# Kernel tuning notes

Measured on AMD Instinct MI355X. Metric: run time of the kernel, lower is better.

The kernel has to match this reference:

```python
import jax, jax.numpy as jnp
import numpy as np

B, N, D = 64, 256, 1024
E_T, E_C, TOP_K = 4, 4, 2
E = E_T + E_C
HT = 4 * N      # token-mixer hidden
HC = 4 * D      # channel-mixer hidden
HM = 4 * D      # mlp hidden
EPS = 1e-6


def _ln(x):
    mu = jnp.mean(x, axis=-1, keepdims=True)
    var = jnp.mean(jnp.square(x - mu), axis=-1, keepdims=True)
    return (x - mu) * jax.lax.rsqrt(var + EPS)


def _gelu(x):
    return jax.nn.gelu(x, approximate=True)


def _modulate(x, shift, scale):
    return x * (1.0 + scale[:, None, :]) + shift[:, None, :]


def setup_inputs() -> dict:
    key = jax.random.key(0)
    ks = jax.random.split(key, 20)
    def rn(k, shape, fan_in):
        return (jax.random.normal(k, shape, dtype=jnp.float32) / np.sqrt(fan_in)).astype(jnp.float32)
    return {
        "x": jax.random.normal(ks[0], (B, N, D), dtype=jnp.float32),
        "c": jax.random.normal(ks[1], (B, D), dtype=jnp.float32),
        "w_ada": rn(ks[2], (D, 6 * D), D),
        "b_ada": jnp.zeros((6 * D,), jnp.float32),
        "w_router": rn(ks[3], (D, E), D),
        "tm_w1": rn(ks[4], (E_T, N, HT), N),
        "tm_b1": jnp.zeros((E_T, HT), jnp.float32),
        "tm_w2": rn(ks[5], (E_T, HT, N), HT),
        "tm_b2": jnp.zeros((E_T, N), jnp.float32),
        "cm_w1": rn(ks[6], (E_C, D, HC), D),
        "cm_b1": jnp.zeros((E_C, HC), jnp.float32),
        "cm_w2": rn(ks[7], (E_C, HC, D), HC),
        "cm_b2": jnp.zeros((E_C, D), jnp.float32),
        "mlp_w1": rn(ks[8], (D, HM), D),
        "mlp_b1": jnp.zeros((HM,), jnp.float32),
        "mlp_w2": rn(ks[9], (HM, D), HM),
        "mlp_b2": jnp.zeros((D,), jnp.float32),
    }


def _mixer(h, w_router, tm_w1, tm_b1, tm_w2, tm_b2, cm_w1, cm_b1, cm_w2, cm_b2):
    # per-sample routing on mean-pooled tokens
    r_in = jnp.mean(h, axis=1)                         # (B, D)
    logits = r_in @ w_router                            # (B, E)
    probs = jax.nn.softmax(logits, axis=-1)
    tw, ti = jax.lax.top_k(probs, TOP_K)                # (B, K)
    tw = tw / jnp.sum(tw, axis=-1, keepdims=True)
    # combine weights: (B, E), zero for non-selected experts
    combine = jnp.zeros((h.shape[0], E), h.dtype).at[jnp.arange(h.shape[0])[:, None], ti].add(tw)
    out = jnp.zeros_like(h)
    hT = jnp.swapaxes(h, 1, 2)                          # (B, D, N)
    for e in range(E_T):
        hid = _gelu(jnp.einsum('bdn,nh->bdh', hT, tm_w1[e]) + tm_b1[e])
        oe = jnp.einsum('bdh,hn->bdn', hid, tm_w2[e]) + tm_b2[e]
        out = out + combine[:, e, None, None] * jnp.swapaxes(oe, 1, 2)
    for e in range(E_C):
        hid = _gelu(jnp.einsum('bnd,dh->bnh', h, cm_w1[e]) + cm_b1[e])
        oe = jnp.einsum('bnh,hd->bnd', hid, cm_w2[e]) + cm_b2[e]
        out = out + combine[:, E_T + e, None, None] * oe
    # aux load-balancing loss (top-1 assignment fraction x mean probs)
    frac = jnp.mean(jax.nn.one_hot(ti[:, 0], E, dtype=probs.dtype), axis=0)
    aux = E * jnp.sum(jnp.mean(probs, axis=0) * frac)
    return out, aux


def reference(x, c, w_ada, b_ada, w_router, tm_w1, tm_b1, tm_w2, tm_b2,
              cm_w1, cm_b1, cm_w2, cm_b2, mlp_w1, mlp_b1, mlp_w2, mlp_b2):
    mod = jax.nn.silu(c) @ w_ada + b_ada                # (B, 6D)
    s_msa, sc_msa, g_msa, s_mlp, sc_mlp, g_mlp = jnp.split(mod, 6, axis=1)
    h = _modulate(_ln(x), s_msa, sc_msa)
    mix, aux = _mixer(h, w_router, tm_w1, tm_b1, tm_w2, tm_b2, cm_w1, cm_b1, cm_w2, cm_b2)
    x = x + g_msa[:, None, :] * mix
    h2 = _modulate(_ln(x), s_mlp, sc_mlp)
    m = _gelu(h2 @ mlp_w1 + mlp_b1) @ mlp_w2 + mlp_b2
    x = x + g_mlp[:, None, :] * m
    return x, aux
```

## Files before the change

kernel.cpp:

```cpp
#include <hip/hip_runtime.h>
#include <stdint.h>

typedef unsigned short u16;
typedef __attribute__((ext_vector_type(8))) __bf16 bf16x8;
typedef __attribute__((ext_vector_type(4))) float f32x4;

#define DEV static __device__ __forceinline__

#define VMW8 asm volatile("s_waitcnt vmcnt(8)" ::: "memory")
#define VMW4 asm volatile("s_waitcnt vmcnt(4)" ::: "memory")
#define VMW0 asm volatile("s_waitcnt vmcnt(0)" ::: "memory")
#define LGK0 asm volatile("s_waitcnt lgkmcnt(0)" ::: "memory")

DEV u16 f2b(float f) {
  uint32_t u = __builtin_bit_cast(uint32_t, f);
  u += 0x7fffu + ((u >> 16) & 1u);
  return (u16)(u >> 16);
}
DEV float gelu_f(float x) {
  return 0.5f * x * (1.0f + tanhf(0.7978845608028654f * (x + 0.044715f * x * x * x)));
}
DEV void async_cp16(const void* g, void* l) {
  __builtin_amdgcn_global_load_lds(
      (const __attribute__((address_space(1))) unsigned int*)g,
      (__attribute__((address_space(3))) unsigned int*)l, 16, 0, 0);
}

DEV int xcd_work(void) {
  int nwg = gridDim.x * gridDim.y;
  int hid = blockIdx.x + blockIdx.y * gridDim.x;
  int cpx = nwg >> 3;
  return (hid & 7) * cpx + (hid >> 3);
}

DEV void gemm_tile(const u16* __restrict__ A, int lda,
                   const u16* __restrict__ B, int ldb, int K,
                   u16* As, u16* Bs, f32x4 acc[4][4]) {
  const int tid = threadIdx.x;
  const int w = tid >> 6;
  const int L = tid & 63;
  const int sr = L >> 2;
  const int sk = (L & 3) * 8;
  const int fm = L & 15;
  const int fk = (L >> 4) * 8;
  const u16* ga0 = A + (size_t)(w * 32 + sr) * lda + sk;
  const u16* ga1 = ga0 + 16 * (size_t)lda;
  const u16* gb0 = B + (size_t)(w * 32 + sr) * ldb + sk;
  const u16* gb1 = gb0 + 16 * (size_t)ldb;
  const int lofs = w * 1024 + L * 8;
  const int nst = K >> 5;

  VMW0;
  __syncthreads();

  {
    u16* la = As + lofs; u16* lb = Bs + lofs;
    async_cp16(ga0, la); async_cp16(ga1, la + 512);
    async_cp16(gb0, lb); async_cp16(gb1, lb + 512);
    la += 4096; lb += 4096;
    async_cp16(ga0 + 32, la); async_cp16(ga1 + 32, la + 512);
    async_cp16(gb0 + 32, lb); async_cp16(gb1 + 32, lb + 512);
  }
  int s0 = 0, s1 = 4096, s2 = 8192;
  for (int t = 0; t < nst; ++t) {
    if (t + 2 < nst) {
      const int kt = (t + 2) * 32;
      u16* la = As + s2 + lofs; u16* lb = Bs + s2 + lofs;
      async_cp16(ga0 + kt, la); async_cp16(ga1 + kt, la + 512);
      async_cp16(gb0 + kt, lb); async_cp16(gb1 + kt, lb + 512);
      VMW8;
    } else if (t + 1 < nst) {
      VMW4;
    } else {
      VMW0;
    }
    __builtin_amdgcn_s_barrier();
    const u16* fa = As + s0 + ((w & 1) * 64 + fm) * 32 + fk;
    const u16* fb = Bs + s0 + ((w >> 1) * 64 + fm) * 32 + fk;
    bf16x8 av[4], bv[4];
#pragma unroll
    for (int i = 0; i < 4; ++i) {
      av[i] = *(const bf16x8*)(fa + i * 512);
      bv[i] = *(const bf16x8*)(fb + i * 512);
    }
#pragma unroll
    for (int i = 0; i < 4; ++i)
#pragma unroll
      for (int j = 0; j < 4; ++j)
        acc[i][j] = __builtin_amdgcn_mfma_f32_16x16x32_bf16(av[i], bv[j], acc[i][j], 0, 0, 0);
    LGK0;
    __builtin_amdgcn_s_barrier();
    __builtin_amdgcn_sched_barrier(0);
    const int tmp = s0; s0 = s1; s1 = s2; s2 = tmp;
  }
}

DEV void zero_acc(f32x4 acc[4][4]) {
  f32x4 z = {0.f, 0.f, 0.f, 0.f};
#pragma unroll
  for (int i = 0; i < 4; ++i)
#pragma unroll
    for (int j = 0; j < 4; ++j) acc[i][j] = z;
}

__global__ void k_diag(float* out, float v) {
  if (threadIdx.x == 0 && blockIdx.x == 0) out[0] = v;
}

struct TDesc { const float* src; long dstOff; int R, C, tileStart, tilesX; };
struct TArgs { TDesc d[17]; int n; };

__global__ __launch_bounds__(256) void k_transpose(TArgs a, u16* __restrict__ ws) {
  __shared__ float tl[32][33];
  int bid = blockIdx.x;
  int di = 0;
  for (int i = 1; i < a.n; ++i) di = (bid >= a.d[i].tileStart) ? i : di;
  TDesc dd = a.d[di];
  int lt = bid - dd.tileStart;
  int tx = lt % dd.tilesX, ty = lt / dd.tilesX;
  int cc = threadIdx.x & 31, rr = threadIdx.x >> 5;
  const float* sp = dd.src + (size_t)(ty * 32) * dd.C + tx * 32;
#pragma unroll
  for (int i = 0; i < 4; ++i) tl[rr + 8 * i][cc] = sp[(size_t)(rr + 8 * i) * dd.C + cc];
  __syncthreads();
  u16* dp = ws + dd.dstOff + (size_t)(tx * 32) * dd.R + ty * 32;
#pragma unroll
  for (int i = 0; i < 4; ++i) dp[(size_t)(rr + 8 * i) * dd.R + cc] = f2b(tl[cc][rr + 8 * i]);
}

__global__ __launch_bounds__(256) void k_silu(const float* __restrict__ c, u16* __restrict__ cs) {
  int row = blockIdx.x, t = threadIdx.x;
  float4 v = {0.f, 0.f, 0.f, 0.f};
  if (row < 64) v = ((const float4*)(c + (size_t)row * 1024))[t];
  ushort4 o;
  o.x = f2b(v.x / (1.f + expf(-v.x)));
  o.y = f2b(v.y / (1.f + expf(-v.y)));
  o.z = f2b(v.z / (1.f + expf(-v.z)));
  o.w = f2b(v.w / (1.f + expf(-v.w)));
  ((ushort4*)(cs + (size_t)row * 1024))[t] = o;
}

__global__ __launch_bounds__(256) void k_ada(const u16* __restrict__ cs, const u16* __restrict__ wT,
                                             const float* __restrict__ bada, float* __restrict__ modp) {
  __shared__ u16 As[12288] __attribute__((aligned(16)));
  __shared__ u16 Bs[12288] __attribute__((aligned(16)));
  int tn = blockIdx.x;
  f32x4 acc[4][4]; zero_acc(acc);
  gemm_tile(cs, 1024, wT + (size_t)tn * 131072, 1024, 1024, As, Bs, acc);
  const int tid = threadIdx.x, w = tid >> 6, L = tid & 63;
  const int rb = (w & 1) * 64 + ((L >> 4) << 2), cb = (w >> 1) * 64 + (L & 15);
#pragma unroll
  for (int i = 0; i < 4; ++i)
#pragma unroll
    for (int j = 0; j < 4; ++j) {
      int col = tn * 128 + cb + j * 16;
      float bv = bada[col];
#pragma unroll
      for (int r = 0; r < 4; ++r) {
        int row = rb + i * 16 + r;
        modp[(size_t)row * 6144 + col] = acc[i][j][r] + bv;
      }
    }
}

__global__ __launch_bounds__(256) void k_ln(const float* __restrict__ xin, const float* __restrict__ modp,
                                            u16* __restrict__ hout, float* __restrict__ stats,
                                            int shOff, int scOff) {
  int n = blockIdx.x, b = blockIdx.y, t = threadIdx.x;
  const float* xr = xin + ((size_t)b * 256 + n) * 1024;
  float4 v = ((const float4*)xr)[t];
  float s = v.x + v.y + v.z + v.w;
  float s2 = v.x * v.x + v.y * v.y + v.z * v.z + v.w * v.w;
#pragma unroll
  for (int o = 32; o; o >>= 1) { s += __shfl_down(s, o); s2 += __shfl_down(s2, o); }
  __shared__ float red[8];
  int wv = t >> 6, l = t & 63;
  if (l == 0) { red[wv] = s; red[4 + wv] = s2; }
  __syncthreads();
  float S = red[0] + red[1] + red[2] + red[3];
  float S2 = red[4] + red[5] + red[6] + red[7];
  float mu = S * (1.f / 1024.f);
  float var = S2 * (1.f / 1024.f) - mu * mu;
  float rstd = rsqrtf(var + 1e-6f);
  if (stats != nullptr && t == 0) { stats[b * 256 + n] = mu; stats[16384 + b * 256 + n] = rstd; }
  float4 sh = ((const float4*)(modp + b * 6144 + shOff))[t];
  float4 sc = ((const float4*)(modp + b * 6144 + scOff))[t];
  ushort4 o;
  o.x = f2b(((v.x - mu) * rstd) * (1.f + sc.x) + sh.x);
  o.y = f2b(((v.y - mu) * rstd) * (1.f + sc.y) + sh.y);
  o.z = f2b(((v.z - mu) * rstd) * (1.f + sc.z) + sh.z);
  o.w = f2b(((v.w - mu) * rstd) * (1.f + sc.w) + sh.w);
  ((ushort4*)(hout + ((size_t)b * 256 + n) * 1024))[t] = o;
}

__global__ __launch_bounds__(256) void k_htrans(const u16* __restrict__ h, u16* __restrict__ hT) {
  __shared__ u16 tl[32][33];
  int b = blockIdx.z, d0 = blockIdx.x * 32, n0 = blockIdx.y * 32;
  int c = threadIdx.x & 31, r = threadIdx.x >> 5;
  const u16* src = h + (size_t)b * 262144;
#pragma unroll
  for (int i = 0; i < 4; ++i) tl[r + 8 * i][c] = src[(size_t)(n0 + r + 8 * i) * 1024 + d0 + c];
  __syncthreads();
  u16* dst = hT + (size_t)b * 262144;
#pragma unroll
  for (int i = 0; i < 4; ++i) dst[(size_t)(d0 + r + 8 * i) * 256 + n0 + c] = tl[c][r + 8 * i];
}

__global__ __launch_bounds__(256) void k_rin(const float* __restrict__ x, const float* __restrict__ lns,
                                             const float* __restrict__ modp, float* __restrict__ rin) {
  int b = blockIdx.y, d = blockIdx.x * 256 + threadIdx.x;
  const float* xp = x + (size_t)b * 262144 + d;
  const float* mu = lns + b * 256;
  const float* rs = lns + 16384 + b * 256;
  float s = 0.f;
  for (int n = 0; n < 256; ++n) s += (xp[(size_t)n * 1024] - mu[n]) * rs[n];
  float sc = modp[b * 6144 + 1024 + d], sh = modp[b * 6144 + d];
  rin[b * 1024 + d] = (1.f + sc) * (s * (1.f / 256.f)) + sh;
}

__global__ __launch_bounds__(256) void k_router(const float* __restrict__ rin, const float* __restrict__ wr,
                                                float* __restrict__ probs, float* __restrict__ tw,
                                                int* __restrict__ ti, int* __restrict__ top1) {
  __shared__ float red[256][8];
  int b = blockIdx.x, t = threadIdx.x;
  float a[8];
#pragma unroll
  for (int e = 0; e < 8; ++e) a[e] = 0.f;
  for (int d = t; d < 1024; d += 256) {
    float rv = rin[b * 1024 + d];
    const float* wp = wr + d * 8;
#pragma unroll
    for (int e = 0; e < 8; ++e) a[e] += rv * wp[e];
  }
#pragma unroll
  for (int e = 0; e < 8; ++e) red[t][e] = a[e];
  __syncthreads();
  for (int s = 128; s > 0; s >>= 1) {
    if (t < s)
#pragma unroll
      for (int e = 0; e < 8; ++e) red[t][e] += red[t + s][e];
    __syncthreads();
  }
  if (t == 0) {
    float p[8];
    float m = -1e30f;
    for (int e = 0; e < 8; ++e) m = fmaxf(m, red[0][e]);
    float sum = 0.f;
    for (int e = 0; e < 8; ++e) { p[e] = expf(red[0][e] - m); sum += p[e]; }
    float inv = 1.f / sum;
    for (int e = 0; e < 8; ++e) p[e] *= inv;
    int i1 = 0;
    for (int e = 1; e < 8; ++e) if (p[e] > p[i1]) i1 = e;
    int i2 = -1; float bv = -1e30f;
    for (int e = 0; e < 8; ++e) if (e != i1 && p[e] > bv) { bv = p[e]; i2 = e; }
    float ss = p[i1] + p[i2];
    ti[b * 2] = i1; ti[b * 2 + 1] = i2;
    tw[b * 2] = p[i1] / ss; tw[b * 2 + 1] = p[i2] / ss;
    top1[b] = i1;
    for (int e = 0; e < 8; ++e) probs[b * 8 + e] = p[e];
  }
}

__global__ void k_aux(const float* __restrict__ probs, const int* __restrict__ top1,
                      float* __restrict__ auxout) {
  if (threadIdx.x != 0) return;
  float mp[8], fr[8];
  for (int e = 0; e < 8; ++e) { mp[e] = 0.f; fr[e] = 0.f; }
  for (int b = 0; b < 64; ++b) {
    for (int e = 0; e < 8; ++e) mp[e] += probs[b * 8 + e];
    fr[top1[b]] += 1.f;
  }
  float aux = 0.f;
  for (int e = 0; e < 8; ++e) aux += (mp[e] * (1.f / 64.f)) * (fr[e] * (1.f / 64.f));
  auxout[0] = 8.f * aux;
}

__global__ __launch_bounds__(256) void k_gemm1(const u16* __restrict__ h, const u16* __restrict__ hT,
                                               const u16* __restrict__ tmw1T, const u16* __restrict__ cmw1T,
                                               const float* __restrict__ tm_b1, const float* __restrict__ cm_b1,
                                               const int* __restrict__ ti, u16* __restrict__ hid, int slot0) {
  __shared__ u16 As[12288] __attribute__((aligned(16)));
  __shared__ u16 Bs[12288] __attribute__((aligned(16)));
  const int wrk = xcd_work();
  int tile = wrk & 63;
  int ly = wrk >> 6;
  int slot = slot0 + ly;
  int b = slot >> 1;
  int e = ti[slot];
  f32x4 acc[4][4]; zero_acc(acc);
  const int tid = threadIdx.x, w = tid >> 6, L = tid & 63;
  const int rb = (w & 1) * 64 + ((L >> 4) << 2), cb = (w >> 1) * 64 + (L & 15);
  u16* outp = hid + (size_t)ly * 1048576;
  if (e < 4) {
    int tm = tile >> 3, tn = tile & 7;
    gemm_tile(hT + (size_t)b * 262144 + (size_t)tm * 128 * 256, 256,
              tmw1T + (size_t)e * 262144 + (size_t)tn * 128 * 256, 256, 256, As, Bs, acc);
    const float* bias = tm_b1 + e * 1024 + tn * 128;
#pragma unroll
    for (int i = 0; i < 4; ++i)
#pragma unroll
      for (int j = 0; j < 4; ++j) {
        int col = cb + j * 16;
        float bv = bias[col];
#pragma unroll
        for (int r = 0; r < 4; ++r) {
          int row = tm * 128 + rb + i * 16 + r;
          outp[(size_t)row * 1024 + tn * 128 + col] = f2b(gelu_f(acc[i][j][r] + bv));
        }
      }
  } else {
    int ec = e - 4;
    int tm = tile >> 5, tn = tile & 31;
    gemm_tile(h + (size_t)b * 262144 + (size_t)tm * 128 * 1024, 1024,
              cmw1T + (size_t)ec * 4194304 + (size_t)tn * 128 * 1024, 1024, 1024, As, Bs, acc);
    const float* bias = cm_b1 + ec * 4096 + tn * 128;
#pragma unroll
    for (int i = 0; i < 4; ++i)
#pragma unroll
      for (int j = 0; j < 4; ++j) {
        int col = cb + j * 16;
        float bv = bias[col];
#pragma unroll
        for (int r = 0; r < 4; ++r) {
          int row = tm * 128 + rb + i * 16 + r;
          outp[(size_t)row * 4096 + tn * 128 + col] = f2b(gelu_f(acc[i][j][r] + bv));
        }
      }
  }
}

__global__ __launch_bounds__(256) void k_gemm2(const u16* __restrict__ hid,
                                               const u16* __restrict__ tmw2T, const u16* __restrict__ cmw2T,
                                               const float* __restrict__ tm_b2, const float* __restrict__ cm_b2,
                                               const int* __restrict__ ti, const float* __restrict__ tw,
                                               const float* __restrict__ x, const float* __restrict__ modp,
                                               float* __restrict__ x1, int b0) {
  __shared__ u16 As[12288] __attribute__((aligned(16)));
  __shared__ u16 Bs[12288] __attribute__((aligned(16)));
  const int wrk = xcd_work();
  int tm = (wrk & 15) >> 3, tn = wrk & 7;
  int ly = wrk >> 4;
  int b = b0 + ly;
  int e0 = ti[b * 2], e1 = ti[b * 2 + 1];
  float w0 = tw[b * 2], w1v = tw[b * 2 + 1];
  f32x4 acc[4][4]; zero_acc(acc);
  const int tid = threadIdx.x, w = tid >> 6, L = tid & 63;
  const int rb = (w & 1) * 64 + ((L >> 4) << 2), cb = (w >> 1) * 64 + (L & 15);
  const u16* hid0 = hid + (size_t)(2 * ly) * 1048576;
  const u16* hid1 = hid0 + 1048576;
  if (e0 < 4)
    gemm_tile(tmw2T + (size_t)e0 * 262144 + (size_t)tm * 128 * 1024, 1024,
              hid0 + (size_t)tn * 128 * 1024, 1024, 1024, As, Bs, acc);
  else
    gemm_tile(hid0 + (size_t)tm * 128 * 4096, 4096,
              cmw2T + (size_t)(e0 - 4) * 4194304 + (size_t)tn * 128 * 4096, 4096, 4096, As, Bs, acc);
  float ratio = w0 / w1v;
#pragma unroll
  for (int i = 0; i < 4; ++i)
#pragma unroll
    for (int j = 0; j < 4; ++j)
#pragma unroll
      for (int r = 0; r < 4; ++r) {
        int rowg = tm * 128 + rb + i * 16 + r;
        int colg = tn * 128 + cb + j * 16;
        float bv = (e0 < 4) ? tm_b2[e0 * 256 + rowg] : cm_b2[(e0 - 4) * 1024 + colg];
        acc[i][j][r] = (acc[i][j][r] + bv) * ratio;
      }
  if (e1 < 4)
    gemm_tile(tmw2T + (size_t)e1 * 262144 + (size_t)tm * 128 * 1024, 1024,
              hid1 + (size_t)tn * 128 * 1024, 1024, 1024, As, Bs, acc);
  else
    gemm_tile(hid1 + (size_t)tm * 128 * 4096, 4096,
              cmw2T + (size_t)(e1 - 4) * 4194304 + (size_t)tn * 128 * 4096, 4096, 4096, As, Bs, acc);
  const float* xrow = x + (size_t)b * 262144;
  const float* gm = modp + b * 6144 + 2048;
  float* orow = x1 + (size_t)b * 262144;
#pragma unroll
  for (int i = 0; i < 4; ++i)
#pragma unroll
    for (int j = 0; j < 4; ++j)
#pragma unroll
      for (int r = 0; r < 4; ++r) {
        int rowg = tm * 128 + rb + i * 16 + r;
        int colg = tn * 128 + cb + j * 16;
        float bv = (e1 < 4) ? tm_b2[e1 * 256 + rowg] : cm_b2[(e1 - 4) * 1024 + colg];
        float val = w1v * (acc[i][j][r] + bv);
        size_t idx = (size_t)rowg * 1024 + colg;
        orow[idx] = xrow[idx] + gm[colg] * val;
      }
}

__global__ __launch_bounds__(256) void k_mlp1(const u16* __restrict__ h2, const u16* __restrict__ w1T,
                                              const float* __restrict__ b1, u16* __restrict__ mhid, int r0) {
  __shared__ u16 As[12288] __attribute__((aligned(16)));
  __shared__ u16 Bs[12288] __attribute__((aligned(16)));
  const int wrk = xcd_work();
  int tn = wrk & 31, tm = wrk >> 5;
  f32x4 acc[4][4]; zero_acc(acc);
  gemm_tile(h2 + (size_t)(r0 + tm * 128) * 1024, 1024, w1T + (size_t)tn * 131072, 1024, 1024, As, Bs, acc);
  const int tid = threadIdx.x, w = tid >> 6, L = tid & 63;
  const int rb = (w & 1) * 64 + ((L >> 4) << 2), cb = (w >> 1) * 64 + (L & 15);
  const float* bias = b1 + tn * 128;
#pragma unroll
  for (int i = 0; i < 4; ++i)
#pragma unroll
    for (int j = 0; j < 4; ++j) {
      int col = cb + j * 16;
      float bv = bias[col];
#pragma unroll
      for (int r = 0; r < 4; ++r) {
        int row = tm * 128 + rb + i * 16 + r;
        mhid[(size_t)row * 4096 + tn * 128 + col] = f2b(gelu_f(acc[i][j][r] + bv));
      }
    }
}

__global__ __launch_bounds__(256) void k_mlp2(const u16* __restrict__ mhid, const u16* __restrict__ w2T,
                                              const float* __restrict__ b2, const float* __restrict__ modp,
                                              float* __restrict__ xio, int r0) {
  __shared__ u16 As[12288] __attribute__((aligned(16)));
  __shared__ u16 Bs[12288] __attribute__((aligned(16)));
  const int wrk = xcd_work();
  int tn = wrk & 7, tm = wrk >> 3;
  f32x4 acc[4][4]; zero_acc(acc);
  gemm_tile(mhid + (size_t)tm * 524288, 4096, w2T + (size_t)tn * 524288, 4096, 4096, As, Bs, acc);
  const int tid = threadIdx.x, w = tid >> 6, L = tid & 63;
  const int rb = (w & 1) * 64 + ((L >> 4) << 2), cb = (w >> 1) * 64 + (L & 15);
#pragma unroll
  for (int i = 0; i < 4; ++i)
#pragma unroll
    for (int j = 0; j < 4; ++j) {
      int col = tn * 128 + cb + j * 16;
      float bv = b2[col];
#pragma unroll
      for (int r = 0; r < 4; ++r) {
        int gr = r0 + tm * 128 + rb + i * 16 + r;
        int bq = gr >> 8;
        size_t idx = (size_t)gr * 1024 + col;
        xio[idx] = xio[idx] + modp[bq * 6144 + 5120 + col] * (acc[i][j][r] + bv);
      }
    }
}

extern "C" void kernel_launch(void* const* d_in, const int* in_sizes, int n_in,
                              void* d_out, int out_size, void* d_ws, size_t ws_size,
                              hipStream_t stream) {
  (void)in_sizes; (void)n_in; (void)out_size;
  const float* x        = (const float*)d_in[0];
  const float* c        = (const float*)d_in[1];
  const float* w_ada    = (const float*)d_in[2];
  const float* b_ada    = (const float*)d_in[3];
  const float* w_router = (const float*)d_in[4];
  const float* tm_w1    = (const float*)d_in[5];
  const float* tm_b1    = (const float*)d_in[6];
  const float* tm_w2    = (const float*)d_in[7];
  const float* tm_b2    = (const float*)d_in[8];
  const float* cm_w1    = (const float*)d_in[9];
  const float* cm_b1    = (const float*)d_in[10];
  const float* cm_w2    = (const float*)d_in[11];
  const float* cm_b2    = (const float*)d_in[12];
  const float* mlp_w1   = (const float*)d_in[13];
  const float* mlp_b1   = (const float*)d_in[14];
  const float* mlp_w2   = (const float*)d_in[15];
  const float* mlp_b2   = (const float*)d_in[16];

  u16* ws16 = (u16*)d_ws;
  char* wsb = (char*)d_ws;
  u16* tmw1T = ws16;
  u16* tmw2T = ws16 + 1048576L;
  u16* cmw1T = ws16 + 2097152L;
  u16* cmw2T = ws16 + 18874368L;
  u16* csilu = ws16 + 35651584L;
  u16* h     = ws16 + 35782656L;
  u16* hT    = ws16 + 52559872L;
  u16* mw1T  = ws16 + 52559872L;
  u16* mw2T  = ws16 + 56754176L;
  float* modp  = (float*)(wsb + 138674176L);
  float* rin   = (float*)(wsb + 141819904L);
  float* probs = (float*)(wsb + 142082048L);
  float* twp   = (float*)(wsb + 142084096L);
  int*   tip   = (int*)(wsb + 142084608L);
  int*   top1p = (int*)(wsb + 142085120L);
  float* lns   = (float*)(wsb + 142085376L);
  const size_t FIXED_END = 142216448ULL;
  u16* tailb = ws16 + FIXED_END / 2;
  float* x1 = (float*)d_out;

  if (ws_size < FIXED_END + 12582912ULL) {
    k_diag<<<1, 64, 0, stream>>>((float*)d_out, (float)(ws_size >> 20));
    return;
  }
  size_t tail = ws_size - FIXED_END;
  int C = 64;
  while ((size_t)C * 4194304ULL > tail) C >>= 1;
  int R = 16384;
  while ((size_t)R * 8192ULL > tail) R >>= 1;

  TArgs t1; int k = 0, start = 0;
#define ADD_T(TA, SRC, DST, RR, CC)                                       \
  do {                                                                    \
    TA.d[k].src = (SRC); TA.d[k].dstOff = (DST);                          \
    TA.d[k].R = (RR); TA.d[k].C = (CC);                                   \
    TA.d[k].tileStart = start; TA.d[k].tilesX = (CC) / 32;                \
    start += ((RR) / 32) * ((CC) / 32); ++k;                              \
  } while (0)
  ADD_T(t1, w_ada, (long)(FIXED_END / 2), 1024, 6144);
  for (int e = 0; e < 4; ++e) ADD_T(t1, tm_w1 + (long)e * 262144, 0L + (long)e * 262144, 256, 1024);
  for (int e = 0; e < 4; ++e) ADD_T(t1, tm_w2 + (long)e * 262144, 1048576L + (long)e * 262144, 1024, 256);
  for (int e = 0; e < 4; ++e) ADD_T(t1, cm_w1 + (long)e * 4194304, 2097152L + (long)e * 4194304, 1024, 4096);
  for (int e = 0; e < 4; ++e) ADD_T(t1, cm_w2 + (long)e * 4194304, 18874368L + (long)e * 4194304, 4096, 1024);
  t1.n = k;
  int t1_tiles = start;

  TArgs t2; k = 0; start = 0;
  ADD_T(t2, mlp_w1, 52559872L, 1024, 4096);
  ADD_T(t2, mlp_w2, 56754176L, 4096, 1024);
  t2.n = k;
  int t2_tiles = start;
#undef ADD_T

  k_transpose<<<dim3(t1_tiles), dim3(256), 0, stream>>>(t1, ws16);
  k_silu<<<dim3(128), dim3(256), 0, stream>>>(c, csilu);
  k_ada<<<dim3(48), dim3(256), 0, stream>>>(csilu, tailb, b_ada, modp);
  k_ln<<<dim3(256, 64), dim3(256), 0, stream>>>(x, modp, h, lns, 0, 1024);
  k_htrans<<<dim3(32, 8, 64), dim3(256), 0, stream>>>(h, hT);
  k_rin<<<dim3(4, 64), dim3(256), 0, stream>>>(x, lns, modp, rin);
  k_router<<<dim3(64), dim3(256), 0, stream>>>(rin, w_router, probs, twp, tip, top1p);
  k_aux<<<dim3(1), dim3(64), 0, stream>>>(probs, top1p, (float*)d_out + 16777216L);
  for (int b0 = 0; b0 < 64; b0 += C) {
    k_gemm1<<<dim3(64, 2 * C), dim3(256), 0, stream>>>(h, hT, tmw1T, cmw1T, tm_b1, cm_b1, tip, tailb, 2 * b0);
    k_gemm2<<<dim3(16, C), dim3(256), 0, stream>>>(tailb, tmw2T, cmw2T, tm_b2, cm_b2, tip, twp, x, modp, x1, b0);
  }
  k_transpose<<<dim3(t2_tiles), dim3(256), 0, stream>>>(t2, ws16);
  k_ln<<<dim3(256, 64), dim3(256), 0, stream>>>(x1, modp, h, nullptr, 3072, 4096);
  for (int r0 = 0; r0 < 16384; r0 += R) {
    k_mlp1<<<dim3(32, R / 128), dim3(256), 0, stream>>>(h, mw1T, mlp_b1, tailb, r0);
    k_mlp2<<<dim3(8, R / 128), dim3(256), 0, stream>>>(tailb, mw2T, mlp_b2, modp, x1, r0);
  }
}
```

Before: 1.928 ms.

## Split-K expert and MLP down-projections with atomic accumulation into residual

The expert down-projection kernel now launches one block per (slot, tile, K-half) instead of one block per sample that runs both experts in sequence. Each block atomically adds its gated, weighted partial sum into x1, which is pre-seeded with a copy of x. The MLP second GEMM is likewise split into two K halves with atomic adds into the residual. This multiplies the block count, to fill the GPU better and shorten the serial per-block K loops. In exchange it adds atomic traffic, an extra full-tensor copy, and a summation order that is no longer deterministic.

```diff
diff --git a/kernel.cpp b/kernel.cpp
--- a/kernel.cpp
+++ b/kernel.cpp
@@ -26,9 +26,9 @@
       (__attribute__((address_space(3))) unsigned int*)l, 16, 0, 0);
 }
 
-DEV int xcd_work(void) {
-  int nwg = gridDim.x * gridDim.y;
-  int hid = blockIdx.x + blockIdx.y * gridDim.x;
+DEV int xcd_work3(void) {
+  int nwg = gridDim.x * gridDim.y * gridDim.z;
+  int hid = blockIdx.x + gridDim.x * (blockIdx.y + gridDim.y * blockIdx.z);
   int cpx = nwg >> 3;
   return (hid & 7) * cpx + (hid >> 3);
 }
@@ -105,6 +105,11 @@
 
 __global__ void k_diag(float* out, float v) {
   if (threadIdx.x == 0 && blockIdx.x == 0) out[0] = v;
+}
+
+__global__ __launch_bounds__(256) void k_copy(const float* __restrict__ src, float* __restrict__ dst) {
+  size_t i = (size_t)blockIdx.x * 256 + threadIdx.x;
+  ((float4*)dst)[i] = ((const float4*)src)[i];
 }
 
 struct TDesc { const float* src; long dstOff; int R, C, tileStart, tilesX; };
@@ -281,7 +286,7 @@
                                                const int* __restrict__ ti, u16* __restrict__ hid, int slot0) {
   __shared__ u16 As[12288] __attribute__((aligned(16)));
   __shared__ u16 Bs[12288] __attribute__((aligned(16)));
-  const int wrk = xcd_work();
+  const int wrk = xcd_work3();
   int tile = wrk & 63;
   int ly = wrk >> 6;
   int slot = slot0 + ly;
@@ -333,28 +338,33 @@
                                                const u16* __restrict__ tmw2T, const u16* __restrict__ cmw2T,
                                                const float* __restrict__ tm_b2, const float* __restrict__ cm_b2,
                                                const int* __restrict__ ti, const float* __restrict__ tw,
-                                               const float* __restrict__ x, const float* __restrict__ modp,
-                                               float* __restrict__ x1, int b0) {
+                                               const float* __restrict__ modp,
+                                               float* __restrict__ x1, int slot0) {
   __shared__ u16 As[12288] __attribute__((aligned(16)));
   __shared__ u16 Bs[12288] __attribute__((aligned(16)));
-  const int wrk = xcd_work();
-  int tm = (wrk & 15) >> 3, tn = wrk & 7;
-  int ly = wrk >> 4;
-  int b = b0 + ly;
-  int e0 = ti[b * 2], e1 = ti[b * 2 + 1];
-  float w0 = tw[b * 2], w1v = tw[b * 2 + 1];
+  const int wrk = xcd_work3();
+  int tile = wrk & 15;
+  int kh = (wrk >> 4) & 1;
+  int ly = wrk >> 5;
+  int tm = tile >> 3, tn = tile & 7;
+  int slot = slot0 + ly;
+  int b = slot >> 1;
+  int e = ti[slot];
+  float we = tw[slot];
   f32x4 acc[4][4]; zero_acc(acc);
   const int tid = threadIdx.x, w = tid >> 6, L = tid & 63;
   const int rb = (w & 1) * 64 + ((L >> 4) << 2), cb = (w >> 1) * 64 + (L & 15);
-  const u16* hid0 = hid + (size_t)(2 * ly) * 1048576;
-  const u16* hid1 = hid0 + 1048576;
-  if (e0 < 4)
-    gemm_tile(tmw2T + (size_t)e0 * 262144 + (size_t)tm * 128 * 1024, 1024,
-              hid0 + (size_t)tn * 128 * 1024, 1024, 1024, As, Bs, acc);
-  else
-    gemm_tile(hid0 + (size_t)tm * 128 * 4096, 4096,
-              cmw2T + (size_t)(e0 - 4) * 4194304 + (size_t)tn * 128 * 4096, 4096, 4096, As, Bs, acc);
-  float ratio = w0 / w1v;
+  const u16* hidS = hid + (size_t)ly * 1048576;
+  if (e < 4) {
+    gemm_tile(tmw2T + (size_t)e * 262144 + (size_t)tm * 128 * 1024 + (size_t)kh * 512, 1024,
+              hidS + (size_t)tn * 128 * 1024 + (size_t)kh * 512, 1024, 512, As, Bs, acc);
+  } else {
+    gemm_tile(hidS + (size_t)tm * 128 * 4096 + (size_t)kh * 2048, 4096,
+              cmw2T + (size_t)(e - 4) * 4194304 + (size_t)tn * 128 * 4096 + (size_t)kh * 2048, 4096,
+              2048, As, Bs, acc);
+  }
+  const float* gm = modp + b * 6144 + 2048;
+  float* orow = x1 + (size_t)b * 262144;
 #pragma unroll
   for (int i = 0; i < 4; ++i)
 #pragma unroll
@@ -363,30 +373,11 @@
       for (int r = 0; r < 4; ++r) {
         int rowg = tm * 128 + rb + i * 16 + r;
         int colg = tn * 128 + cb + j * 16;
-        float bv = (e0 < 4) ? tm_b2[e0 * 256 + rowg] : cm_b2[(e0 - 4) * 1024 + colg];
-        acc[i][j][r] = (acc[i][j][r] + bv) * ratio;
-      }
-  if (e1 < 4)
-    gemm_tile(tmw2T + (size_t)e1 * 262144 + (size_t)tm * 128 * 1024, 1024,
-              hid1 + (size_t)tn * 128 * 1024, 1024, 1024, As, Bs, acc);
-  else
-    gemm_tile(hid1 + (size_t)tm * 128 * 4096, 4096,
-              cmw2T + (size_t)(e1 - 4) * 4194304 + (size_t)tn * 128 * 4096, 4096, 4096, As, Bs, acc);
-  const float* xrow = x + (size_t)b * 262144;
-  const float* gm = modp + b * 6144 + 2048;
-  float* orow = x1 + (size_t)b * 262144;
-#pragma unroll
-  for (int i = 0; i < 4; ++i)
-#pragma unroll
-    for (int j = 0; j < 4; ++j)
-#pragma unroll
-      for (int r = 0; r < 4; ++r) {
-        int rowg = tm * 128 + rb + i * 16 + r;
-        int colg = tn * 128 + cb + j * 16;
-        float bv = (e1 < 4) ? tm_b2[e1 * 256 + rowg] : cm_b2[(e1 - 4) * 1024 + colg];
-        float val = w1v * (acc[i][j][r] + bv);
-        size_t idx = (size_t)rowg * 1024 + colg;
-        orow[idx] = xrow[idx] + gm[colg] * val;
+        float bv = (kh == 0)
+                       ? ((e < 4) ? tm_b2[e * 256 + rowg] : cm_b2[(e - 4) * 1024 + colg])
+                       : 0.f;
+        float term = gm[colg] * (we * (acc[i][j][r] + bv));
+        unsafeAtomicAdd(&orow[(size_t)rowg * 1024 + colg], term);
       }
 }
 
@@ -394,7 +385,7 @@
                                               const float* __restrict__ b1, u16* __restrict__ mhid, int r0) {
   __shared__ u16 As[12288] __attribute__((aligned(16)));
   __shared__ u16 Bs[12288] __attribute__((aligned(16)));
-  const int wrk = xcd_work();
+  const int wrk = xcd_work3();
   int tn = wrk & 31, tm = wrk >> 5;
   f32x4 acc[4][4]; zero_acc(acc);
   gemm_tile(h2 + (size_t)(r0 + tm * 128) * 1024, 1024, w1T + (size_t)tn * 131072, 1024, 1024, As, Bs, acc);
@@ -420,10 +411,11 @@
                                               float* __restrict__ xio, int r0) {
   __shared__ u16 As[12288] __attribute__((aligned(16)));
   __shared__ u16 Bs[12288] __attribute__((aligned(16)));
-  const int wrk = xcd_work();
-  int tn = wrk & 7, tm = wrk >> 3;
+  const int wrk = xcd_work3();
+  int tn = wrk & 7, kh = (wrk >> 3) & 1, tm = wrk >> 4;
   f32x4 acc[4][4]; zero_acc(acc);
-  gemm_tile(mhid + (size_t)tm * 524288, 4096, w2T + (size_t)tn * 524288, 4096, 4096, As, Bs, acc);
+  gemm_tile(mhid + (size_t)tm * 524288 + (size_t)kh * 2048, 4096,
+            w2T + (size_t)tn * 524288 + (size_t)kh * 2048, 4096, 2048, As, Bs, acc);
   const int tid = threadIdx.x, w = tid >> 6, L = tid & 63;
   const int rb = (w & 1) * 64 + ((L >> 4) << 2), cb = (w >> 1) * 64 + (L & 15);
 #pragma unroll
@@ -431,13 +423,13 @@
 #pragma unroll
     for (int j = 0; j < 4; ++j) {
       int col = tn * 128 + cb + j * 16;
-      float bv = b2[col];
+      float bv = (kh == 0) ? b2[col] : 0.f;
 #pragma unroll
       for (int r = 0; r < 4; ++r) {
         int gr = r0 + tm * 128 + rb + i * 16 + r;
         int bq = gr >> 8;
-        size_t idx = (size_t)gr * 1024 + col;
-        xio[idx] = xio[idx] + modp[bq * 6144 + 5120 + col] * (acc[i][j][r] + bv);
+        float term = modp[bq * 6144 + 5120 + col] * (acc[i][j][r] + bv);
+        unsafeAtomicAdd(&xio[(size_t)gr * 1024 + col], term);
       }
     }
 }
@@ -520,6 +512,7 @@
 #undef ADD_T
 
   k_transpose<<<dim3(t1_tiles), dim3(256), 0, stream>>>(t1, ws16);
+  k_copy<<<dim3(16384), dim3(256), 0, stream>>>(x, x1);
   k_silu<<<dim3(128), dim3(256), 0, stream>>>(c, csilu);
   k_ada<<<dim3(48), dim3(256), 0, stream>>>(csilu, tailb, b_ada, modp);
   k_ln<<<dim3(256, 64), dim3(256), 0, stream>>>(x, modp, h, lns, 0, 1024);
@@ -529,12 +522,12 @@
   k_aux<<<dim3(1), dim3(64), 0, stream>>>(probs, top1p, (float*)d_out + 16777216L);
   for (int b0 = 0; b0 < 64; b0 += C) {
     k_gemm1<<<dim3(64, 2 * C), dim3(256), 0, stream>>>(h, hT, tmw1T, cmw1T, tm_b1, cm_b1, tip, tailb, 2 * b0);
-    k_gemm2<<<dim3(16, C), dim3(256), 0, stream>>>(tailb, tmw2T, cmw2T, tm_b2, cm_b2, tip, twp, x, modp, x1, b0);
+    k_gemm2<<<dim3(16, 2 * C, 2), dim3(256), 0, stream>>>(tailb, tmw2T, cmw2T, tm_b2, cm_b2, tip, twp, modp, x1, 2 * b0);
   }
   k_transpose<<<dim3(t2_tiles), dim3(256), 0, stream>>>(t2, ws16);
   k_ln<<<dim3(256, 64), dim3(256), 0, stream>>>(x1, modp, h, nullptr, 3072, 4096);
   for (int r0 = 0; r0 < 16384; r0 += R) {
     k_mlp1<<<dim3(32, R / 128), dim3(256), 0, stream>>>(h, mw1T, mlp_b1, tailb, r0);
-    k_mlp2<<<dim3(8, R / 128), dim3(256), 0, stream>>>(tailb, mw2T, mlp_b2, modp, x1, r0);
-  }
-}
+    k_mlp2<<<dim3(16, R / 128), dim3(256), 0, stream>>>(tailb, mw2T, mlp_b2, modp, x1, r0);
+  }
+}
```

Result: slower. 2.089 ms (+8.3%).
